# Kernel optimization log

Hardware: AMD Instinct MI355X
Metric: run time of the kernel (lower is better)

## Reference

```python
import jax, jax.numpy as jnp
import numpy as np

BETA = 0.9
THR = 1.0
ALPHA = 2.0  # snntorch surrogate.atan default

@jax.custom_vjp
def atan_spike(x):
    return (x > 0).astype(x.dtype)

def _atan_fwd(x):
    return atan_spike(x), x

def _atan_bwd(x, g):
    # snntorch ATan surrogate: alpha/2 / (1 + (pi/2 * alpha * x)^2)
    return (g * (ALPHA / 2.0) / (1.0 + (jnp.pi / 2.0 * ALPHA * x) ** 2),)

atan_spike.defvjp(_atan_fwd, _atan_bwd)

def setup_inputs() -> dict:
    key = jax.random.key(0)
    k = jax.random.split(key, 5)
    B, T, C, H, W = 128, 25, 3, 64, 64
    F, HID, O = C * H * W, 2048, 2
    bound1 = 1.0 / np.sqrt(F)
    boundo = 1.0 / np.sqrt(HID)
    return {
        "x": jax.random.normal(k[0], (B, T, C, H, W), jnp.float32),
        "W1": jax.random.uniform(k[1], (HID, F), jnp.float32, -bound1, bound1),
        "b1": jax.random.uniform(k[2], (HID,), jnp.float32, -bound1, bound1),
        "Wo": jax.random.uniform(k[3], (O, HID), jnp.float32, -boundo, boundo),
        "bo": jax.random.uniform(k[4], (O,), jnp.float32, -boundo, boundo),
    }

def reference(x, W1, b1, Wo, bo):
    B, T = x.shape[0], x.shape[1]
    HID, O = W1.shape[0], Wo.shape[0]
    xf = x.reshape(B, T, -1).transpose(1, 0, 2)  # [T, B, F]
    # fc1 for all timesteps at once (input is fixed per step)
    h_all = jnp.einsum('tbf,hf->tbh', xf, W1) + b1  # [T, B, HID]

    def step(carry, h):
        mem1, memo = carry
        # snntorch Leaky (reset_mechanism='subtract'): reset from previous mem
        r1 = atan_spike(mem1 - THR)
        mem1 = BETA * mem1 + h - r1 * THR
        s1 = atan_spike(mem1 - THR)
        o = s1 @ Wo.T + bo
        ro = atan_spike(memo - THR)
        memo = BETA * memo + o - ro * THR
        so = atan_spike(memo - THR)
        return (mem1, memo), so

    init = (jnp.zeros((B, HID), x.dtype), jnp.zeros((B, O), x.dtype))
    (_, _), spk_rec = jax.lax.scan(step, init, h_all)
    # train=False path: sum of output spikes over time
    return spk_rec.sum(axis=0)  # [B, O]
```

## Files before the change

kernel.cpp:

```cpp
#include <hip/hip_runtime.h>


#define T_STEPS 25
#define B_SZ    128
#define F_SZ    12288
#define HID_SZ  2048
#define KT      384
#define M_PAD   3328
#define UPB     156
#define PART_STRIDE ((size_t)M_PAD * HID_SZ)

typedef __attribute__((ext_vector_type(8))) _Float16 f16x8;
typedef __attribute__((ext_vector_type(4))) float f32x4;
typedef __attribute__((ext_vector_type(16))) float f32x16;

__device__ __forceinline__ void g2l16(const void* g, void* l) {
  __builtin_amdgcn_global_load_lds(
      (const __attribute__((address_space(1))) void*)g,
      (__attribute__((address_space(3))) void*)l, 16, 0, 0);
}

__device__ __forceinline__ void split8(f32x4 v0, f32x4 v1,
                                       f16x8& hi, f16x8& lo, float sc) {
#pragma unroll
  for (int j = 0; j < 4; ++j) {
    float a = v0[j] * sc;
    _Float16 h = (_Float16)a;
    hi[j] = h;
    lo[j] = (_Float16)(a - (float)h);
    float b = v1[j] * sc;
    _Float16 h2 = (_Float16)b;
    hi[4 + j] = h2;
    lo[4 + j] = (_Float16)(b - (float)h2);
  }
}

__global__ __launch_bounds__(512, 1) void gemm_persist_kernel(
    const float* __restrict__ x, const float* __restrict__ W1,
    float* __restrict__ parts) {
  __shared__ __align__(16) char lds[131072];
  const int tid = threadIdx.x;
  const int l = tid & 63;
  const int w = tid >> 6;
  const int wm = w >> 2;
  const int wn = w & 3;

  const int swz = ((blockIdx.x & 7) << 5) + (blockIdx.x >> 3);

  const int srow = tid >> 3;
  const int sof = (((tid & 7) ^ (srow & 7)) << 4);

  const int lxor = l & 7;
  const int klo = (l >> 5) * 2;
  const int arow = (wm * 128 + (l & 31)) * 128;
  const int brow = (wn * 64 + (l & 31)) * 128;

  int u = swz * UPB;
  const int u1 = u + UPB;

  while (u < u1) {
    const int mnt = u / 384;
    const int kt0 = u - mnt * 384;
    const int rem_t = 384 - kt0, rem_u = u1 - u;
    const int seg = rem_t < rem_u ? rem_t : rem_u;
    const int ktN = kt0 + seg;
    const int mt = mnt >> 3;
    const int nt = mnt & 7;

    int pm0 = mt * 256 + 0 * 64 + srow; pm0 = pm0 > 3199 ? 3199 : pm0;
    int pm1 = mt * 256 + 1 * 64 + srow; pm1 = pm1 > 3199 ? 3199 : pm1;
    int pm2 = mt * 256 + 2 * 64 + srow; pm2 = pm2 > 3199 ? 3199 : pm2;
    int pm3 = mt * 256 + 3 * 64 + srow; pm3 = pm3 > 3199 ? 3199 : pm3;
    const char* aB0 = (const char*)(x + ((size_t)((pm0 & 127) * T_STEPS + (pm0 >> 7))) * F_SZ) + sof;
    const char* aB1 = (const char*)(x + ((size_t)((pm1 & 127) * T_STEPS + (pm1 >> 7))) * F_SZ) + sof;
    const char* aB2 = (const char*)(x + ((size_t)((pm2 & 127) * T_STEPS + (pm2 >> 7))) * F_SZ) + sof;
    const char* aB3 = (const char*)(x + ((size_t)((pm3 & 127) * T_STEPS + (pm3 >> 7))) * F_SZ) + sof;
    const char* bB0 = (const char*)(W1 + (size_t)(nt * 256 +   0 + srow) * F_SZ) + sof;
    const char* bB1 = (const char*)(W1 + (size_t)(nt * 256 +  64 + srow) * F_SZ) + sof;
    const char* bB2 = (const char*)(W1 + (size_t)(nt * 256 + 128 + srow) * F_SZ) + sof;
    const char* bB3 = (const char*)(W1 + (size_t)(nt * 256 + 192 + srow) * F_SZ) + sof;

#define STAGE(ktx)                                                     \
    do {                                                               \
      char* d_ = (char*)lds + ((ktx) & 1) * 65536 + tid * 16;          \
      const int ko_ = (ktx) * 128;                                     \
      g2l16(aB0 + ko_, d_);         g2l16(bB0 + ko_, d_ + 32768);      \
      g2l16(aB1 + ko_, d_ + 8192);  g2l16(bB1 + ko_, d_ + 40960);      \
      g2l16(aB2 + ko_, d_ + 16384); g2l16(bB2 + ko_, d_ + 49152);      \
      g2l16(aB3 + ko_, d_ + 24576); g2l16(bB3 + ko_, d_ + 57344);      \
    } while (0)

    f32x16 acc[4][2];
#pragma unroll
    for (int i = 0; i < 4; ++i)
#pragma unroll
      for (int j = 0; j < 2; ++j)
#pragma unroll
        for (int r = 0; r < 16; ++r) acc[i][j][r] = 0.f;

    STAGE(kt0);

    for (int kt = kt0; kt < ktN; ++kt) {
      __syncthreads();
      if (kt + 1 < ktN) STAGE(kt + 1);

      const char* la = (const char*)lds + (kt & 1) * 65536;
      const char* lb = la + 32768;

#pragma unroll
      for (int ks = 0; ks < 2; ++ks) {
        const int s0 = ks * 4 + klo;
        const int o0 = (s0 ^ lxor) << 4;
        const int o1 = ((s0 + 1) ^ lxor) << 4;
        f16x8 ah[4], al[4];
#pragma unroll
        for (int mf = 0; mf < 4; ++mf) {
          f32x4 v0 = *(const f32x4*)(la + arow + mf * 4096 + o0);
          f32x4 v1 = *(const f32x4*)(la + arow + mf * 4096 + o1);
          split8(v0, v1, ah[mf], al[mf], 1.0f);
        }
#pragma unroll
        for (int nf = 0; nf < 2; ++nf) {
          f32x4 u0 = *(const f32x4*)(lb + brow + nf * 4096 + o0);
          f32x4 u1 = *(const f32x4*)(lb + brow + nf * 4096 + o1);
          f16x8 bh, bl;
          split8(u0, u1, bh, bl, 128.0f);
          __builtin_amdgcn_s_setprio(1);
#pragma unroll
          for (int mf = 0; mf < 4; ++mf) {
            acc[mf][nf] = __builtin_amdgcn_mfma_f32_32x32x16_f16(ah[mf], bh, acc[mf][nf], 0, 0, 0);
            acc[mf][nf] = __builtin_amdgcn_mfma_f32_32x32x16_f16(ah[mf], bl, acc[mf][nf], 0, 0, 0);
            acc[mf][nf] = __builtin_amdgcn_mfma_f32_32x32x16_f16(al[mf], bh, acc[mf][nf], 0, 0, 0);
          }
          __builtin_amdgcn_s_setprio(0);
        }
      }
    }

    const int slot = swz - (mnt * 384) / UPB;
    float* dst = parts + (size_t)slot * PART_STRIDE;
    const int row0 = mt * 256 + wm * 128 + ((l >> 5) << 2);
    const int col0 = nt * 256 + wn * 64 + (l & 31);
#pragma unroll
    for (int nf = 0; nf < 2; ++nf)
#pragma unroll
      for (int mf = 0; mf < 4; ++mf)
#pragma unroll
        for (int r = 0; r < 16; ++r) {
          const int row = row0 + mf * 32 + (r & 3) + ((r >> 2) << 3);
          dst[(size_t)row * HID_SZ + col0 + nf * 32] = acc[mf][nf][r];
        }
    u += seg;
    __syncthreads();
#undef STAGE
  }
}

__global__ __launch_bounds__(256) void gemm_h_kernel(
    const float* __restrict__ x, const float* __restrict__ W1,
    const float* __restrict__ b1, float* __restrict__ h_all) {
  __shared__ float As[16][128];
  __shared__ float Bs[16][128];
  const int tid = threadIdx.x;
  const int tx = tid & 15;
  const int ty = tid >> 4;
  const int m0 = blockIdx.x * 128;
  const int n0 = blockIdx.y * 128;
  const int lrow = tid >> 1;
  const int lcol = (tid & 1) * 8;
  const int gm = m0 + lrow;
  const int bb = gm & (B_SZ - 1);
  const int tt = gm >> 7;
  const float* aptr = x + ((size_t)bb * T_STEPS + tt) * F_SZ + lcol;
  const float* bptr = W1 + (size_t)(n0 + lrow) * F_SZ + lcol;
  float acc[8][8];
#pragma unroll
  for (int i = 0; i < 8; ++i)
#pragma unroll
    for (int j = 0; j < 8; ++j) acc[i][j] = 0.f;
  for (int k0 = 0; k0 < F_SZ; k0 += 16) {
    float4 av0 = *(const float4*)(aptr + k0);
    float4 av1 = *(const float4*)(aptr + k0 + 4);
    float4 bv0 = *(const float4*)(bptr + k0);
    float4 bv1 = *(const float4*)(bptr + k0 + 4);
    As[lcol + 0][lrow] = av0.x; As[lcol + 1][lrow] = av0.y;
    As[lcol + 2][lrow] = av0.z; As[lcol + 3][lrow] = av0.w;
    As[lcol + 4][lrow] = av1.x; As[lcol + 5][lrow] = av1.y;
    As[lcol + 6][lrow] = av1.z; As[lcol + 7][lrow] = av1.w;
    Bs[lcol + 0][lrow] = bv0.x; Bs[lcol + 1][lrow] = bv0.y;
    Bs[lcol + 2][lrow] = bv0.z; Bs[lcol + 3][lrow] = bv0.w;
    Bs[lcol + 4][lrow] = bv1.x; Bs[lcol + 5][lrow] = bv1.y;
    Bs[lcol + 6][lrow] = bv1.z; Bs[lcol + 7][lrow] = bv1.w;
    __syncthreads();
#pragma unroll
    for (int k = 0; k < 16; ++k) {
      float4 a0 = *(const float4*)&As[k][ty * 8];
      float4 a1 = *(const float4*)&As[k][ty * 8 + 4];
      float4 q0 = *(const float4*)&Bs[k][tx * 8];
      float4 q1 = *(const float4*)&Bs[k][tx * 8 + 4];
      float ar[8] = {a0.x, a0.y, a0.z, a0.w, a1.x, a1.y, a1.z, a1.w};
      float br[8] = {q0.x, q0.y, q0.z, q0.w, q1.x, q1.y, q1.z, q1.w};
#pragma unroll
      for (int i = 0; i < 8; ++i)
#pragma unroll
        for (int j = 0; j < 8; ++j)
          acc[i][j] = fmaf(ar[i], br[j], acc[i][j]);
    }
    __syncthreads();
  }
#pragma unroll
  for (int i = 0; i < 8; ++i) {
    const int gm2 = m0 + ty * 8 + i;
    float* orow = h_all + (size_t)gm2 * HID_SZ + n0 + tx * 8;
    const float* brow = b1 + n0 + tx * 8;
#pragma unroll
    for (int j = 0; j < 8; ++j) orow[j] = acc[i][j] + brow[j];
  }
}

__global__ __launch_bounds__(256) void lif_hidden_kernel(
    const float* __restrict__ parts, const float* __restrict__ b1,
    const float* __restrict__ Wo, float* __restrict__ oc, int mode) {
  const int b = blockIdx.x & 127;
  const int half = blockIdx.x >> 7;
  const int tid = threadIdx.x;
  const int h0 = half * 1024;
  float mem1[4], wo0[4], wo1[4], bv[4];
#pragma unroll
  for (int i = 0; i < 4; ++i) {
    const int hid = h0 + 256 * i + tid;
    mem1[i] = 0.f;
    wo0[i] = Wo[hid];
    wo1[i] = Wo[HID_SZ + hid];
    bv[i] = b1[hid];
  }
  __shared__ float partial[4][2];
  for (int t = 0; t < T_STEPS; ++t) {
    const int row = t * B_SZ + b;
    const size_t rowb = (size_t)row * HID_SZ;
    const int mt8 = (row >> 8) * 8;
    float pr0 = 0.f, pr1 = 0.f;
#pragma unroll
    for (int i = 0; i < 4; ++i) {
      const int hid = h0 + 256 * i + tid;
      const size_t idx = rowb + hid;
      float h;
      if (mode == 2) {
        float s = parts[idx] + parts[idx + PART_STRIDE] +
                  parts[idx + 2 * PART_STRIDE];
        const int k0 = (mt8 + (hid >> 8)) * 384;
        if ((k0 + 383) / UPB - k0 / UPB + 1 == 4)
          s += parts[idx + 3 * PART_STRIDE];
        h = s * 0.0078125f + bv[i];
      } else {
        h = parts[idx];
      }
      float r1 = mem1[i] > 1.0f ? 1.0f : 0.0f;
      float m = 0.9f * mem1[i] + h - r1;
      mem1[i] = m;
      if (m > 1.0f) { pr0 += wo0[i]; pr1 += wo1[i]; }
    }
#pragma unroll
    for (int off = 32; off > 0; off >>= 1) {
      pr0 += __shfl_down(pr0, off);
      pr1 += __shfl_down(pr1, off);
    }
    if ((tid & 63) == 0) { partial[tid >> 6][0] = pr0; partial[tid >> 6][1] = pr1; }
    __syncthreads();
    if (tid == 0) {
      const size_t o = (((size_t)b * 2 + half) * T_STEPS + t) * 2;
      oc[o + 0] = partial[0][0] + partial[1][0] + partial[2][0] + partial[3][0];
      oc[o + 1] = partial[0][1] + partial[1][1] + partial[2][1] + partial[3][1];
    }
    __syncthreads();
  }
}

__global__ __launch_bounds__(128) void lif_out_kernel(
    const float* __restrict__ oc, const float* __restrict__ bo,
    float* __restrict__ out) {
  const int b = threadIdx.x;
  float memo0 = 0.f, memo1 = 0.f, a0 = 0.f, a1 = 0.f;
  const float bo0 = bo[0], bo1 = bo[1];
  for (int t = 0; t < T_STEPS; ++t) {
    const size_t i0 = (((size_t)b * 2 + 0) * T_STEPS + t) * 2;
    const size_t i1 = (((size_t)b * 2 + 1) * T_STEPS + t) * 2;
    float o0 = oc[i0] + oc[i1] + bo0;
    float o1 = oc[i0 + 1] + oc[i1 + 1] + bo1;
    float ro0 = memo0 > 1.0f ? 1.0f : 0.0f;
    float ro1 = memo1 > 1.0f ? 1.0f : 0.0f;
    memo0 = 0.9f * memo0 + o0 - ro0;
    memo1 = 0.9f * memo1 + o1 - ro1;
    a0 += memo0 > 1.0f ? 1.0f : 0.0f;
    a1 += memo1 > 1.0f ? 1.0f : 0.0f;
  }
  out[b * 2 + 0] = a0;
  out[b * 2 + 1] = a1;
}

extern "C" void kernel_launch(void* const* d_in, const int* in_sizes, int n_in,
                              void* d_out, int out_size, void* d_ws, size_t ws_size,
                              hipStream_t stream) {
  const float* x  = (const float*)d_in[0];
  const float* W1 = (const float*)d_in[1];
  const float* b1 = (const float*)d_in[2];
  const float* Wo = (const float*)d_in[3];
  const float* bo = (const float*)d_in[4];
  float* out = (float*)d_out;

  const size_t part_bytes = PART_STRIDE * 4;
  const size_t oc_bytes = (size_t)128 * 2 * T_STEPS * 2 * 4;
  char* ws = (char*)d_ws;
  float* parts = (float*)ws;

  if (ws_size >= 4 * part_bytes + oc_bytes) {
    float* oc = (float*)(ws + 4 * part_bytes);
    gemm_persist_kernel<<<256, 512, 0, stream>>>(x, W1, parts);
    lif_hidden_kernel<<<256, 256, 0, stream>>>(parts, b1, Wo, oc, 2);
    lif_out_kernel<<<1, 128, 0, stream>>>(oc, bo, out);
  } else {
    float* oc = (float*)(ws + part_bytes);
    dim3 grid(25, 16);
    gemm_h_kernel<<<grid, 256, 0, stream>>>(x, W1, b1, parts);
    lif_hidden_kernel<<<256, 256, 0, stream>>>(parts, b1, Wo, oc, 0);
    lif_out_kernel<<<1, 128, 0, stream>>>(oc, bo, out);
  }
}
```

Before: 616.3 us.

## Pre-split W1 into fp16 hi/lo tiles and reorder tile traversal

Adds a pre-pass kernel that converts W1 once per call into scaled fp16 hi/lo pairs stored in an MFMA-friendly tiled layout, so the GEMM loads B fragments directly instead of converting fp32 to split fp16 in its inner loop. The A staging layout is changed to a k-group-major, unswizzled arrangement, and the persistent tile order now iterates m-tiles within each n-tile so blocks sharing W1 tiles run near each other. The reduction kernel's partial-count logic is updated for the new mnt mapping. The cost is an extra kernel launch and about 100MB of extra workspace traffic for the converted weights, plus possible LDS bank conflicts from removing the XOR swizzle.

After: 672.1 us. 9.1% more time.

```diff
diff --git a/kernel.cpp b/kernel.cpp
--- a/kernel.cpp
+++ b/kernel.cpp
@@ -20,23 +20,47 @@
       (__attribute__((address_space(3))) void*)l, 16, 0, 0);
 }
 
-__device__ __forceinline__ void split8(f32x4 v0, f32x4 v1,
-                                       f16x8& hi, f16x8& lo, float sc) {
+__device__ __forceinline__ void split8(f32x4 v0, f32x4 v1, f16x8& hi, f16x8& lo) {
 #pragma unroll
   for (int j = 0; j < 4; ++j) {
-    float a = v0[j] * sc;
-    _Float16 h = (_Float16)a;
+    _Float16 h = (_Float16)v0[j];
     hi[j] = h;
-    lo[j] = (_Float16)(a - (float)h);
-    float b = v1[j] * sc;
-    _Float16 h2 = (_Float16)b;
+    lo[j] = (_Float16)(v0[j] - (float)h);
+    _Float16 h2 = (_Float16)v1[j];
     hi[4 + j] = h2;
-    lo[4 + j] = (_Float16)(b - (float)h2);
+    lo[4 + j] = (_Float16)(v1[j] - (float)h2);
+  }
+}
+
+__global__ __launch_bounds__(256) void conv_w_kernel(
+    const float* __restrict__ W1, char* __restrict__ B2) {
+  const int total = 8 * KT * 256 * 4;
+  for (int i = blockIdx.x * 256 + threadIdx.x; i < total; i += gridDim.x * 256) {
+    const int s = i & 3;
+    const int r = (i >> 2) & 255;
+    const int rest = i >> 10;
+    const int ks = rest % KT;
+    const int nt = rest / KT;
+    const float* src = W1 + ((size_t)(nt * 256 + r)) * F_SZ + ks * 32 + s * 8;
+    float4 v0 = *(const float4*)src;
+    float4 v1 = *(const float4*)(src + 4);
+    float vf[8] = {v0.x, v0.y, v0.z, v0.w, v1.x, v1.y, v1.z, v1.w};
+    f16x8 hi, lo;
+#pragma unroll
+    for (int j = 0; j < 8; ++j) {
+      float vs = vf[j] * 128.0f;
+      _Float16 h = (_Float16)vs;
+      hi[j] = h;
+      lo[j] = (_Float16)(vs - (float)h);
+    }
+    char* chunk = B2 + (size_t)rest * 32768;
+    *(f16x8*)(chunk + s * 4096 + r * 16) = hi;
+    *(f16x8*)(chunk + (s + 4) * 4096 + r * 16) = lo;
   }
 }
 
 __global__ __launch_bounds__(512, 1) void gemm_persist_kernel(
-    const float* __restrict__ x, const float* __restrict__ W1,
+    const float* __restrict__ x, const char* __restrict__ B2,
     float* __restrict__ parts) {
   __shared__ __align__(16) char lds[131072];
   const int tid = threadIdx.x;
@@ -44,16 +68,12 @@
   const int w = tid >> 6;
   const int wm = w >> 2;
   const int wn = w & 3;
+  const int lhalf = l >> 5;
 
   const int swz = ((blockIdx.x & 7) << 5) + (blockIdx.x >> 3);
 
-  const int srow = tid >> 3;
-  const int sof = (((tid & 7) ^ (srow & 7)) << 4);
-
-  const int lxor = l & 7;
-  const int klo = (l >> 5) * 2;
-  const int arow = (wm * 128 + (l & 31)) * 128;
-  const int brow = (wn * 64 + (l & 31)) * 128;
+  const int arow = (wm * 128 + (l & 31)) * 16;
+  const int brow = (wn * 64 + (l & 31)) * 16;
 
   int u = swz * UPB;
   const int u1 = u + UPB;
@@ -64,30 +84,24 @@
     const int rem_t = 384 - kt0, rem_u = u1 - u;
     const int seg = rem_t < rem_u ? rem_t : rem_u;
     const int ktN = kt0 + seg;
-    const int mt = mnt >> 3;
-    const int nt = mnt & 7;
-
-    int pm0 = mt * 256 + 0 * 64 + srow; pm0 = pm0 > 3199 ? 3199 : pm0;
-    int pm1 = mt * 256 + 1 * 64 + srow; pm1 = pm1 > 3199 ? 3199 : pm1;
-    int pm2 = mt * 256 + 2 * 64 + srow; pm2 = pm2 > 3199 ? 3199 : pm2;
-    int pm3 = mt * 256 + 3 * 64 + srow; pm3 = pm3 > 3199 ? 3199 : pm3;
-    const char* aB0 = (const char*)(x + ((size_t)((pm0 & 127) * T_STEPS + (pm0 >> 7))) * F_SZ) + sof;
-    const char* aB1 = (const char*)(x + ((size_t)((pm1 & 127) * T_STEPS + (pm1 >> 7))) * F_SZ) + sof;
-    const char* aB2 = (const char*)(x + ((size_t)((pm2 & 127) * T_STEPS + (pm2 >> 7))) * F_SZ) + sof;
-    const char* aB3 = (const char*)(x + ((size_t)((pm3 & 127) * T_STEPS + (pm3 >> 7))) * F_SZ) + sof;
-    const char* bB0 = (const char*)(W1 + (size_t)(nt * 256 +   0 + srow) * F_SZ) + sof;
-    const char* bB1 = (const char*)(W1 + (size_t)(nt * 256 +  64 + srow) * F_SZ) + sof;
-    const char* bB2 = (const char*)(W1 + (size_t)(nt * 256 + 128 + srow) * F_SZ) + sof;
-    const char* bB3 = (const char*)(W1 + (size_t)(nt * 256 + 192 + srow) * F_SZ) + sof;
-
-#define STAGE(ktx)                                                     \
-    do {                                                               \
-      char* d_ = (char*)lds + ((ktx) & 1) * 65536 + tid * 16;          \
-      const int ko_ = (ktx) * 128;                                     \
-      g2l16(aB0 + ko_, d_);         g2l16(bB0 + ko_, d_ + 32768);      \
-      g2l16(aB1 + ko_, d_ + 8192);  g2l16(bB1 + ko_, d_ + 40960);      \
-      g2l16(aB2 + ko_, d_ + 16384); g2l16(bB2 + ko_, d_ + 49152);      \
-      g2l16(aB3 + ko_, d_ + 24576); g2l16(bB3 + ko_, d_ + 57344);      \
+    const int nt = mnt / 13;
+    const int mt = mnt - nt * 13;
+
+    int m = mt * 256 + (tid & 255);
+    if (m > 3199) m = 3199;
+    const char* aRow = (const char*)(x +
+        ((size_t)((m & 127) * T_STEPS + (m >> 7))) * F_SZ) + ((tid >> 8) << 4);
+    const char* bBase = B2 + (size_t)nt * KT * 32768 + tid * 16;
+
+#define STAGE(ktx)                                                        \
+    do {                                                                  \
+      char* d_ = (char*)lds + ((ktx) & 1) * 65536 + tid * 16;             \
+      const char* as_ = aRow + (ktx) * 128;                               \
+      const char* bs_ = bBase + (size_t)(ktx) * 32768;                    \
+      g2l16(as_, d_);              g2l16(as_ + 32, d_ + 8192);            \
+      g2l16(as_ + 64, d_ + 16384); g2l16(as_ + 96, d_ + 24576);           \
+      g2l16(bs_, d_ + 32768);          g2l16(bs_ + 8192, d_ + 40960);     \
+      g2l16(bs_ + 16384, d_ + 49152);  g2l16(bs_ + 24576, d_ + 57344);    \
     } while (0)
 
     f32x16 acc[4][2];
@@ -109,22 +123,19 @@
 
 #pragma unroll
       for (int ks = 0; ks < 2; ++ks) {
-        const int s0 = ks * 4 + klo;
-        const int o0 = (s0 ^ lxor) << 4;
-        const int o1 = ((s0 + 1) ^ lxor) << 4;
+        const int g = ks * 2 + lhalf;
+        const int aBase = g * 8192 + arow;
         f16x8 ah[4], al[4];
 #pragma unroll
         for (int mf = 0; mf < 4; ++mf) {
-          f32x4 v0 = *(const f32x4*)(la + arow + mf * 4096 + o0);
-          f32x4 v1 = *(const f32x4*)(la + arow + mf * 4096 + o1);
-          split8(v0, v1, ah[mf], al[mf], 1.0f);
+          f32x4 v0 = *(const f32x4*)(la + aBase + mf * 512);
+          f32x4 v1 = *(const f32x4*)(la + aBase + 4096 + mf * 512);
+          split8(v0, v1, ah[mf], al[mf]);
         }
 #pragma unroll
         for (int nf = 0; nf < 2; ++nf) {
-          f32x4 u0 = *(const f32x4*)(lb + brow + nf * 4096 + o0);
-          f32x4 u1 = *(const f32x4*)(lb + brow + nf * 4096 + o1);
-          f16x8 bh, bl;
-          split8(u0, u1, bh, bl, 128.0f);
+          f16x8 bh = *(const f16x8*)(lb + g * 4096 + brow + nf * 512);
+          f16x8 bl = *(const f16x8*)(lb + 16384 + g * 4096 + brow + nf * 512);
           __builtin_amdgcn_s_setprio(1);
 #pragma unroll
           for (int mf = 0; mf < 4; ++mf) {
@@ -139,7 +150,7 @@
 
     const int slot = swz - (mnt * 384) / UPB;
     float* dst = parts + (size_t)slot * PART_STRIDE;
-    const int row0 = mt * 256 + wm * 128 + ((l >> 5) << 2);
+    const int row0 = mt * 256 + wm * 128 + (lhalf << 2);
     const int col0 = nt * 256 + wn * 64 + (l & 31);
 #pragma unroll
     for (int nf = 0; nf < 2; ++nf)
@@ -238,7 +249,7 @@
   for (int t = 0; t < T_STEPS; ++t) {
     const int row = t * B_SZ + b;
     const size_t rowb = (size_t)row * HID_SZ;
-    const int mt8 = (row >> 8) * 8;
+    const int mt = row >> 8;
     float pr0 = 0.f, pr1 = 0.f;
 #pragma unroll
     for (int i = 0; i < 4; ++i) {
@@ -248,7 +259,8 @@
       if (mode == 2) {
         float s = parts[idx] + parts[idx + PART_STRIDE] +
                   parts[idx + 2 * PART_STRIDE];
-        const int k0 = (mt8 + (hid >> 8)) * 384;
+        const int mnt = (hid >> 8) * 13 + mt;
+        const int k0 = mnt * 384;
         if ((k0 + 383) / UPB - k0 / UPB + 1 == 4)
           s += parts[idx + 3 * PART_STRIDE];
         h = s * 0.0078125f + bv[i];
@@ -309,13 +321,16 @@
   float* out = (float*)d_out;
 
   const size_t part_bytes = PART_STRIDE * 4;
+  const size_t b2_bytes = (size_t)8 * KT * 32768;
   const size_t oc_bytes = (size_t)128 * 2 * T_STEPS * 2 * 4;
   char* ws = (char*)d_ws;
   float* parts = (float*)ws;
 
-  if (ws_size >= 4 * part_bytes + oc_bytes) {
-    float* oc = (float*)(ws + 4 * part_bytes);
-    gemm_persist_kernel<<<256, 512, 0, stream>>>(x, W1, parts);
+  if (ws_size >= 4 * part_bytes + b2_bytes + oc_bytes) {
+    char* B2 = ws + 4 * part_bytes;
+    float* oc = (float*)(B2 + b2_bytes);
+    conv_w_kernel<<<2048, 256, 0, stream>>>(W1, B2);
+    gemm_persist_kernel<<<256, 512, 0, stream>>>(x, B2, parts);
     lif_hidden_kernel<<<256, 256, 0, stream>>>(parts, b1, Wo, oc, 2);
     lif_out_kernel<<<1, 128, 0, stream>>>(oc, bo, out);
   } else {
```
